# Kernel tuning notes

Hardware: AMD Instinct MI355X
Metric: run time of the kernel (lower is better)

Reference implementation:

```python
import jax, jax.numpy as jnp
import numpy as np

B, S, D = 256, 512, 256
ATT = 128

def setup_inputs() -> dict:
    key = jax.random.key(0)
    k1, k2, k3, k4 = jax.random.split(key, 4)
    x = jax.random.normal(k1, (B, S, D), dtype=jnp.float32)
    W = jax.random.normal(k2, (D, ATT), dtype=jnp.float32)
    b = jax.random.normal(k3, (ATT,), dtype=jnp.float32)
    u = jax.random.normal(k4, (ATT, 1), dtype=jnp.float32)
    return {"x": x, "W": W, "b": b, "u": u}

def reference(x, W, b, u):
    # uit: [B, S, ATT]
    uit = jnp.tanh(jnp.einsum('bsd,da->bsa', x, W) + b)
    # scores: [B, S]  (faithful: exp without max-subtraction, as in original)
    ait = jnp.exp(jnp.einsum('bsa,a->bs', uit, u[:, 0]))
    ait = ait / (jnp.sum(ait, axis=1, keepdims=True) + 1e-08)
    # weighted sum over seq -> [B, D]
    return jnp.einsum('bsd,bs->bd', x, ait)
```

## Files before the change

kernel.cpp:

```cpp
#include <hip/hip_runtime.h>
#include <math.h>

typedef _Float16 f16x8 __attribute__((ext_vector_type(8)));
typedef float    f32x4 __attribute__((ext_vector_type(4)));

constexpr int B_ = 256, S_ = 512, D_ = 256, A_ = 128;
constexpr int BS = B_ * S_;

constexpr size_t WH_OFF = (size_t)BS * sizeof(float);
constexpr size_t WL_OFF = WH_OFF + (size_t)D_ * A_ * 2;

__global__ __launch_bounds__(256) void k_packW(const float* __restrict__ W,
                                               _Float16* __restrict__ Wh,
                                               _Float16* __restrict__ Wl)
{
    int tid = blockIdx.x * 256 + threadIdx.x;
    int l  = tid & 63;
    int nf = (tid >> 6) & 7;
    int ks = tid >> 9;
    int n  = nf * 16 + (l & 15);
    int k0 = ks * 32 + ((l >> 4) & 3) * 8;
    f16x8 hi, lo;
#pragma unroll
    for (int i = 0; i < 8; ++i) {
        float v = W[(k0 + i) * A_ + n];
        _Float16 h = (_Float16)v;
        hi[i] = h;
        lo[i] = (_Float16)(v - (float)h);
    }
    *(f16x8*)(Wh + (size_t)tid * 8) = hi;
    *(f16x8*)(Wl + (size_t)tid * 8) = lo;
}

__global__ __launch_bounds__(256, 2) void k_scores(
    const float* __restrict__ x, const _Float16* __restrict__ Wh,
    const _Float16* __restrict__ Wl, const float* __restrict__ bvec,
    const float* __restrict__ u, float* __restrict__ scores)
{
    const int lane = threadIdx.x & 63;
    const int wv   = threadIdx.x >> 6;
    const int row_base = blockIdx.x * 256 + wv * 64;
    const int lr = lane & 15;
    const int lg = lane >> 4;

    const f32x4 vzero = {0.f, 0.f, 0.f, 0.f};
    f32x4 acc[4][8];
#pragma unroll
    for (int mf = 0; mf < 4; ++mf)
#pragma unroll
        for (int nf = 0; nf < 8; ++nf) acc[mf][nf] = vzero;

    for (int ks = 0; ks < 8; ++ks) {
        f16x8 ah[4], al[4];
#pragma unroll
        for (int mf = 0; mf < 4; ++mf) {
            const float* xp = x + (size_t)(row_base + mf * 16 + lr) * D_ + ks * 32 + lg * 8;
            float4 v0 = *(const float4*)xp;
            float4 v1 = *(const float4*)(xp + 4);
            f16x8 h, lo;
            h[0] = (_Float16)v0.x; h[1] = (_Float16)v0.y;
            h[2] = (_Float16)v0.z; h[3] = (_Float16)v0.w;
            h[4] = (_Float16)v1.x; h[5] = (_Float16)v1.y;
            h[6] = (_Float16)v1.z; h[7] = (_Float16)v1.w;
            lo[0] = (_Float16)(v0.x - (float)h[0]); lo[1] = (_Float16)(v0.y - (float)h[1]);
            lo[2] = (_Float16)(v0.z - (float)h[2]); lo[3] = (_Float16)(v0.w - (float)h[3]);
            lo[4] = (_Float16)(v1.x - (float)h[4]); lo[5] = (_Float16)(v1.y - (float)h[5]);
            lo[6] = (_Float16)(v1.z - (float)h[6]); lo[7] = (_Float16)(v1.w - (float)h[7]);
            ah[mf] = h; al[mf] = lo;
        }
        const f16x8* WhB = (const f16x8*)Wh + (size_t)ks * 8 * 64 + lane;
        const f16x8* WlB = (const f16x8*)Wl + (size_t)ks * 8 * 64 + lane;
#pragma unroll
        for (int nf = 0; nf < 8; ++nf) {
            f16x8 bh = WhB[nf * 64];
            f16x8 bl = WlB[nf * 64];
#pragma unroll
            for (int mf = 0; mf < 4; ++mf) {
                acc[mf][nf] = __builtin_amdgcn_mfma_f32_16x16x32_f16(ah[mf], bh, acc[mf][nf], 0, 0, 0);
                acc[mf][nf] = __builtin_amdgcn_mfma_f32_16x16x32_f16(ah[mf], bl, acc[mf][nf], 0, 0, 0);
                acc[mf][nf] = __builtin_amdgcn_mfma_f32_16x16x32_f16(al[mf], bh, acc[mf][nf], 0, 0, 0);
            }
        }
    }

    float bb[8], uu[8];
#pragma unroll
    for (int nf = 0; nf < 8; ++nf) {
        bb[nf] = bvec[nf * 16 + lr];
        uu[nf] = u[nf * 16 + lr];
    }
#pragma unroll
    for (int mf = 0; mf < 4; ++mf) {
#pragma unroll
        for (int r = 0; r < 4; ++r) {
            float s = 0.f;
#pragma unroll
            for (int nf = 0; nf < 8; ++nf)
                s += tanhf(acc[mf][nf][r] + bb[nf]) * uu[nf];
#pragma unroll
            for (int m = 8; m >= 1; m >>= 1)
                s += __shfl_xor(s, m, 64);
            if (lr == 0)
                scores[row_base + mf * 16 + lg * 4 + r] = expf(s);
        }
    }
}

__global__ __launch_bounds__(512) void k_out(
    const float* __restrict__ x, const float* __restrict__ scores,
    float* __restrict__ out)
{
    __shared__ float sc[S_];
    __shared__ float red[8];
    __shared__ float pbuf[8][D_];

    const int t = threadIdx.x, b = blockIdx.x;
    const int lane = t & 63, w = t >> 6;

    float v = scores[(size_t)b * S_ + t];
    sc[t] = v;
    float rv = v;
#pragma unroll
    for (int m = 32; m >= 1; m >>= 1) rv += __shfl_xor(rv, m, 64);
    if (lane == 0) red[w] = rv;
    __syncthreads();

    const float* xp = x + ((size_t)b * S_ + (size_t)w * 64) * D_ + lane * 4;
    float4 a0 = {0.f, 0.f, 0.f, 0.f}, a1 = {0.f, 0.f, 0.f, 0.f};
#pragma unroll 8
    for (int j = 0; j < 64; j += 2) {
        float4 xa = *(const float4*)(xp + (size_t)j * D_);
        float4 xb = *(const float4*)(xp + (size_t)(j + 1) * D_);
        float s0 = sc[w * 64 + j], s1 = sc[w * 64 + j + 1];
        a0.x = fmaf(xa.x, s0, a0.x); a0.y = fmaf(xa.y, s0, a0.y);
        a0.z = fmaf(xa.z, s0, a0.z); a0.w = fmaf(xa.w, s0, a0.w);
        a1.x = fmaf(xb.x, s1, a1.x); a1.y = fmaf(xb.y, s1, a1.y);
        a1.z = fmaf(xb.z, s1, a1.z); a1.w = fmaf(xb.w, s1, a1.w);
    }
    float4 asum = {a0.x + a1.x, a0.y + a1.y, a0.z + a1.z, a0.w + a1.w};
    *(float4*)(&pbuf[w][lane * 4]) = asum;
    __syncthreads();

    if (t < D_) {
        float denom = 0.f;
#pragma unroll
        for (int i = 0; i < 8; ++i) denom += red[i];
        const float inv = 1.0f / (denom + 1e-8f);
        float r = 0.f;
#pragma unroll
        for (int w2 = 0; w2 < 8; ++w2) r += pbuf[w2][t];
        out[b * D_ + t] = r * inv;
    }
}

extern "C" void kernel_launch(void* const* d_in, const int* in_sizes, int n_in,
                              void* d_out, int out_size, void* d_ws, size_t ws_size,
                              hipStream_t stream)
{
    const float* x    = (const float*)d_in[0];
    const float* W    = (const float*)d_in[1];
    const float* bvec = (const float*)d_in[2];
    const float* u    = (const float*)d_in[3];
    float* out = (float*)d_out;

    float*    scores = (float*)d_ws;
    _Float16* Wh     = (_Float16*)((char*)d_ws + WH_OFF);
    _Float16* Wl     = (_Float16*)((char*)d_ws + WL_OFF);

    k_packW <<<16, 256, 0, stream>>>(W, Wh, Wl);
    k_scores<<<BS / 256, 256, 0, stream>>>(x, Wh, Wl, bvec, u, scores);
    k_out   <<<B_, 512, 0, stream>>>(x, scores, out);
}
```

Measured before the change: 253.0 us.

## Keep W fragments in registers, stage x tiles through LDS with prefetch

The scores kernel now keeps each wave's W hi/lo fragments resident in registers. Each wave owns two column fragments and loops over 32-row tiles of x, which are split into fp16 hi/lo and staged through double-synchronised LDS. Global loads for the next tile are issued before the MFMA work on the current one, and per-wave partial dot products are combined through shared memory. tanhf is replaced with an exp-based fast tanh, and k_out is widened to 1024 threads with half the rows per wave, which adds register pressure and more barriers in exchange.

```diff
diff --git a/kernel.cpp b/kernel.cpp
--- a/kernel.cpp
+++ b/kernel.cpp
@@ -9,6 +9,10 @@
 
 constexpr size_t WH_OFF = (size_t)BS * sizeof(float);
 constexpr size_t WL_OFF = WH_OFF + (size_t)D_ * A_ * 2;
+
+__device__ __forceinline__ float tanh_fast(float v) {
+    return 1.0f - 2.0f / (1.0f + __expf(2.0f * v));
+}
 
 __global__ __launch_bounds__(256) void k_packW(const float* __restrict__ W,
                                                _Float16* __restrict__ Wh,
@@ -37,108 +41,159 @@
     const _Float16* __restrict__ Wl, const float* __restrict__ bvec,
     const float* __restrict__ u, float* __restrict__ scores)
 {
-    const int lane = threadIdx.x & 63;
-    const int wv   = threadIdx.x >> 6;
-    const int row_base = blockIdx.x * 256 + wv * 64;
-    const int lr = lane & 15;
-    const int lg = lane >> 4;
-
-    const f32x4 vzero = {0.f, 0.f, 0.f, 0.f};
-    f32x4 acc[4][8];
-#pragma unroll
-    for (int mf = 0; mf < 4; ++mf)
-#pragma unroll
-        for (int nf = 0; nf < 8; ++nf) acc[mf][nf] = vzero;
-
-    for (int ks = 0; ks < 8; ++ks) {
-        f16x8 ah[4], al[4];
-#pragma unroll
-        for (int mf = 0; mf < 4; ++mf) {
-            const float* xp = x + (size_t)(row_base + mf * 16 + lr) * D_ + ks * 32 + lg * 8;
-            float4 v0 = *(const float4*)xp;
-            float4 v1 = *(const float4*)(xp + 4);
-            f16x8 h, lo;
-            h[0] = (_Float16)v0.x; h[1] = (_Float16)v0.y;
-            h[2] = (_Float16)v0.z; h[3] = (_Float16)v0.w;
-            h[4] = (_Float16)v1.x; h[5] = (_Float16)v1.y;
-            h[6] = (_Float16)v1.z; h[7] = (_Float16)v1.w;
-            lo[0] = (_Float16)(v0.x - (float)h[0]); lo[1] = (_Float16)(v0.y - (float)h[1]);
-            lo[2] = (_Float16)(v0.z - (float)h[2]); lo[3] = (_Float16)(v0.w - (float)h[3]);
-            lo[4] = (_Float16)(v1.x - (float)h[4]); lo[5] = (_Float16)(v1.y - (float)h[5]);
-            lo[6] = (_Float16)(v1.z - (float)h[6]); lo[7] = (_Float16)(v1.w - (float)h[7]);
-            ah[mf] = h; al[mf] = lo;
-        }
-        const f16x8* WhB = (const f16x8*)Wh + (size_t)ks * 8 * 64 + lane;
-        const f16x8* WlB = (const f16x8*)Wl + (size_t)ks * 8 * 64 + lane;
-#pragma unroll
-        for (int nf = 0; nf < 8; ++nf) {
-            f16x8 bh = WhB[nf * 64];
-            f16x8 bl = WlB[nf * 64];
-#pragma unroll
-            for (int mf = 0; mf < 4; ++mf) {
-                acc[mf][nf] = __builtin_amdgcn_mfma_f32_16x16x32_f16(ah[mf], bh, acc[mf][nf], 0, 0, 0);
-                acc[mf][nf] = __builtin_amdgcn_mfma_f32_16x16x32_f16(ah[mf], bl, acc[mf][nf], 0, 0, 0);
-                acc[mf][nf] = __builtin_amdgcn_mfma_f32_16x16x32_f16(al[mf], bh, acc[mf][nf], 0, 0, 0);
-            }
-        }
-    }
-
-    float bb[8], uu[8];
-#pragma unroll
-    for (int nf = 0; nf < 8; ++nf) {
-        bb[nf] = bvec[nf * 16 + lr];
-        uu[nf] = u[nf * 16 + lr];
-    }
-#pragma unroll
-    for (int mf = 0; mf < 4; ++mf) {
-#pragma unroll
-        for (int r = 0; r < 4; ++r) {
-            float s = 0.f;
-#pragma unroll
-            for (int nf = 0; nf < 8; ++nf)
-                s += tanhf(acc[mf][nf][r] + bb[nf]) * uu[nf];
-#pragma unroll
-            for (int m = 8; m >= 1; m >>= 1)
-                s += __shfl_xor(s, m, 64);
-            if (lr == 0)
-                scores[row_base + mf * 16 + lg * 4 + r] = expf(s);
-        }
-    }
-}
-
-__global__ __launch_bounds__(512) void k_out(
+    __shared__ _Float16 xh[16 * 64 * 8];
+    __shared__ _Float16 xl[16 * 64 * 8];
+    __shared__ float    part[2][4][32];
+
+    const int t    = threadIdx.x;
+    const int lane = t & 63, wv = t >> 6;
+    const int lr   = lane & 15, lg = lane >> 4;
+    const int brow0 = blockIdx.x * 256;
+
+    f16x8 Bh[8][2], Bl[8][2];
+#pragma unroll
+    for (int ks = 0; ks < 8; ++ks)
+#pragma unroll
+        for (int j = 0; j < 2; ++j) {
+            int nf = wv * 2 + j;
+            Bh[ks][j] = *(const f16x8*)(Wh + ((size_t)(ks * 8 + nf) * 64 + lane) * 8);
+            Bl[ks][j] = *(const f16x8*)(Wl + ((size_t)(ks * 8 + nf) * 64 + lane) * 8);
+        }
+
+    const float bb0 = bvec[(wv * 2 + 0) * 16 + lr], uu0 = u[(wv * 2 + 0) * 16 + lr];
+    const float bb1 = bvec[(wv * 2 + 1) * 16 + lr], uu1 = u[(wv * 2 + 1) * 16 + lr];
+
+    float4 ld[4][2];
+
+#pragma unroll
+    for (int it = 0; it < 4; ++it) {
+        int f = wv * 4 + it;
+        const float* p = x + (size_t)(brow0 + ((f >> 3) << 4) + lr) * D_
+                           + ((f & 7) << 5) + (lg << 3);
+        ld[it][0] = *(const float4*)p;
+        ld[it][1] = *(const float4*)(p + 4);
+    }
+#pragma unroll
+    for (int it = 0; it < 4; ++it) {
+        int f = wv * 4 + it;
+        float v[8] = {ld[it][0].x, ld[it][0].y, ld[it][0].z, ld[it][0].w,
+                      ld[it][1].x, ld[it][1].y, ld[it][1].z, ld[it][1].w};
+        f16x8 hi, lo;
+#pragma unroll
+        for (int i = 0; i < 8; ++i) {
+            _Float16 h = (_Float16)v[i];
+            hi[i] = h; lo[i] = (_Float16)(v[i] - (float)h);
+        }
+        *(f16x8*)&xh[((size_t)f * 64 + lane) * 8] = hi;
+        *(f16x8*)&xl[((size_t)f * 64 + lane) * 8] = lo;
+    }
+
+    for (int tt = 0; tt < 8; ++tt) {
+        __syncthreads();
+        if (tt > 0 && t < 32) {
+            int pp = (tt - 1) & 1;
+            float ss = part[pp][0][t] + part[pp][1][t] + part[pp][2][t] + part[pp][3][t];
+            scores[brow0 + (tt - 1) * 32 + t] = __expf(ss);
+        }
+        if (tt < 7) {
+#pragma unroll
+            for (int it = 0; it < 4; ++it) {
+                int f = wv * 4 + it;
+                const float* p = x + (size_t)(brow0 + (tt + 1) * 32 + ((f >> 3) << 4) + lr) * D_
+                                   + ((f & 7) << 5) + (lg << 3);
+                ld[it][0] = *(const float4*)p;
+                ld[it][1] = *(const float4*)(p + 4);
+            }
+        }
+        f32x4 acc[2][2];
+#pragma unroll
+        for (int mt = 0; mt < 2; ++mt)
+#pragma unroll
+            for (int j = 0; j < 2; ++j) acc[mt][j] = (f32x4){0.f, 0.f, 0.f, 0.f};
+#pragma unroll
+        for (int mt = 0; mt < 2; ++mt)
+#pragma unroll
+            for (int ks = 0; ks < 8; ++ks) {
+                int fi = mt * 8 + ks;
+                f16x8 ah = *(const f16x8*)&xh[((size_t)fi * 64 + lane) * 8];
+                f16x8 al = *(const f16x8*)&xl[((size_t)fi * 64 + lane) * 8];
+                acc[mt][0] = __builtin_amdgcn_mfma_f32_16x16x32_f16(ah, Bh[ks][0], acc[mt][0], 0, 0, 0);
+                acc[mt][0] = __builtin_amdgcn_mfma_f32_16x16x32_f16(ah, Bl[ks][0], acc[mt][0], 0, 0, 0);
+                acc[mt][0] = __builtin_amdgcn_mfma_f32_16x16x32_f16(al, Bh[ks][0], acc[mt][0], 0, 0, 0);
+                acc[mt][1] = __builtin_amdgcn_mfma_f32_16x16x32_f16(ah, Bh[ks][1], acc[mt][1], 0, 0, 0);
+                acc[mt][1] = __builtin_amdgcn_mfma_f32_16x16x32_f16(ah, Bl[ks][1], acc[mt][1], 0, 0, 0);
+                acc[mt][1] = __builtin_amdgcn_mfma_f32_16x16x32_f16(al, Bh[ks][1], acc[mt][1], 0, 0, 0);
+            }
+        const int par = tt & 1;
+#pragma unroll
+        for (int mt = 0; mt < 2; ++mt)
+#pragma unroll
+            for (int r = 0; r < 4; ++r) {
+                float s = tanh_fast(acc[mt][0][r] + bb0) * uu0
+                        + tanh_fast(acc[mt][1][r] + bb1) * uu1;
+                s += __shfl_xor(s, 8, 64);
+                s += __shfl_xor(s, 4, 64);
+                s += __shfl_xor(s, 2, 64);
+                s += __shfl_xor(s, 1, 64);
+                if (lr == 0) part[par][wv][mt * 16 + lg * 4 + r] = s;
+            }
+        __syncthreads();
+        if (tt < 7) {
+#pragma unroll
+            for (int it = 0; it < 4; ++it) {
+                int f = wv * 4 + it;
+                float v[8] = {ld[it][0].x, ld[it][0].y, ld[it][0].z, ld[it][0].w,
+                              ld[it][1].x, ld[it][1].y, ld[it][1].z, ld[it][1].w};
+                f16x8 hi, lo;
+#pragma unroll
+                for (int i = 0; i < 8; ++i) {
+                    _Float16 h = (_Float16)v[i];
+                    hi[i] = h; lo[i] = (_Float16)(v[i] - (float)h);
+                }
+                *(f16x8*)&xh[((size_t)f * 64 + lane) * 8] = hi;
+                *(f16x8*)&xl[((size_t)f * 64 + lane) * 8] = lo;
+            }
+        }
+    }
+    __syncthreads();
+    if (t < 32) {
+        float ss = part[1][0][t] + part[1][1][t] + part[1][2][t] + part[1][3][t];
+        scores[brow0 + 7 * 32 + t] = __expf(ss);
+    }
+}
+
+__global__ __launch_bounds__(1024) void k_out(
     const float* __restrict__ x, const float* __restrict__ scores,
     float* __restrict__ out)
 {
     __shared__ float sc[S_];
     __shared__ float red[8];
-    __shared__ float pbuf[8][D_];
+    __shared__ float pbuf[16][D_];
 
     const int t = threadIdx.x, b = blockIdx.x;
     const int lane = t & 63, w = t >> 6;
 
-    float v = scores[(size_t)b * S_ + t];
-    sc[t] = v;
-    float rv = v;
-#pragma unroll
-    for (int m = 32; m >= 1; m >>= 1) rv += __shfl_xor(rv, m, 64);
-    if (lane == 0) red[w] = rv;
+    if (t < S_) {
+        float v = scores[(size_t)b * S_ + t];
+        sc[t] = v;
+#pragma unroll
+        for (int m = 32; m >= 1; m >>= 1) v += __shfl_xor(v, m, 64);
+        if (lane == 0) red[w] = v;
+    }
     __syncthreads();
 
-    const float* xp = x + ((size_t)b * S_ + (size_t)w * 64) * D_ + lane * 4;
-    float4 a0 = {0.f, 0.f, 0.f, 0.f}, a1 = {0.f, 0.f, 0.f, 0.f};
+    const float* xp = x + ((size_t)b * S_ + (size_t)w * 32) * D_ + lane * 4;
+    f32x4 a = {0.f, 0.f, 0.f, 0.f};
 #pragma unroll 8
-    for (int j = 0; j < 64; j += 2) {
-        float4 xa = *(const float4*)(xp + (size_t)j * D_);
-        float4 xb = *(const float4*)(xp + (size_t)(j + 1) * D_);
-        float s0 = sc[w * 64 + j], s1 = sc[w * 64 + j + 1];
-        a0.x = fmaf(xa.x, s0, a0.x); a0.y = fmaf(xa.y, s0, a0.y);
-        a0.z = fmaf(xa.z, s0, a0.z); a0.w = fmaf(xa.w, s0, a0.w);
-        a1.x = fmaf(xb.x, s1, a1.x); a1.y = fmaf(xb.y, s1, a1.y);
-        a1.z = fmaf(xb.z, s1, a1.z); a1.w = fmaf(xb.w, s1, a1.w);
-    }
-    float4 asum = {a0.x + a1.x, a0.y + a1.y, a0.z + a1.z, a0.w + a1.w};
-    *(float4*)(&pbuf[w][lane * 4]) = asum;
+    for (int j = 0; j < 32; ++j) {
+        float4 xv = *(const float4*)(xp + (size_t)j * D_);
+        float s = sc[w * 32 + j];
+        a[0] = fmaf(xv.x, s, a[0]);
+        a[1] = fmaf(xv.y, s, a[1]);
+        a[2] = fmaf(xv.z, s, a[2]);
+        a[3] = fmaf(xv.w, s, a[3]);
+    }
+    *(f32x4*)&pbuf[w][lane * 4] = a;
     __syncthreads();
 
     if (t < D_) {
@@ -148,7 +203,7 @@
         const float inv = 1.0f / (denom + 1e-8f);
         float r = 0.f;
 #pragma unroll
-        for (int w2 = 0; w2 < 8; ++w2) r += pbuf[w2][t];
+        for (int i = 0; i < 16; ++i) r += pbuf[i][t];
         out[b * D_ + t] = r * inv;
     }
 }
@@ -168,6 +223,6 @@
     _Float16* Wl     = (_Float16*)((char*)d_ws + WL_OFF);
 
     k_packW <<<16, 256, 0, stream>>>(W, Wh, Wl);
-    k_scores<<<BS / 256, 256, 0, stream>>>(x, Wh, Wl, bvec, u, scores);
-    k_out   <<<B_, 512, 0, stream>>>(x, scores, out);
-}
+    k_scores<<<512, 256, 0, stream>>>(x, Wh, Wl, bvec, u, scores);
+    k_out   <<<B_, 1024, 0, stream>>>(x, scores, out);
+}
```

Result: faster. 226.1 us (-10.6%).

## Keep W fragments in registers, stage x via LDS with pipelined prefetch

Applied to the files above, without the earlier changes.

Drops the separate W packing kernel. Each wave of k_scores now splits W into fp16 hi/lo fragments in registers for its own 16 attention columns. Blocks of 512 threads loop over 8 tiles of 32 rows: each tile of x is converted once to hi/lo fp16 and staged in shared memory so all 8 waves reuse it, and the next tile's global loads are issued while the MFMAs run. Per-wave partial scores are reduced across waves through double-buffered shared memory, and tanhf is replaced with an exp-based approximation. This trades extra block syncs and some tanh accuracy for much less per-wave x reloading and conversion, and fewer accumulator registers.

```diff
diff --git a/kernel.cpp b/kernel.cpp
--- a/kernel.cpp
+++ b/kernel.cpp
@@ -7,103 +7,121 @@
 constexpr int B_ = 256, S_ = 512, D_ = 256, A_ = 128;
 constexpr int BS = B_ * S_;
 
-constexpr size_t WH_OFF = (size_t)BS * sizeof(float);
-constexpr size_t WL_OFF = WH_OFF + (size_t)D_ * A_ * 2;
-
-__global__ __launch_bounds__(256) void k_packW(const float* __restrict__ W,
-                                               _Float16* __restrict__ Wh,
-                                               _Float16* __restrict__ Wl)
-{
-    int tid = blockIdx.x * 256 + threadIdx.x;
-    int l  = tid & 63;
-    int nf = (tid >> 6) & 7;
-    int ks = tid >> 9;
-    int n  = nf * 16 + (l & 15);
-    int k0 = ks * 32 + ((l >> 4) & 3) * 8;
-    f16x8 hi, lo;
-#pragma unroll
-    for (int i = 0; i < 8; ++i) {
-        float v = W[(k0 + i) * A_ + n];
-        _Float16 h = (_Float16)v;
-        hi[i] = h;
-        lo[i] = (_Float16)(v - (float)h);
-    }
-    *(f16x8*)(Wh + (size_t)tid * 8) = hi;
-    *(f16x8*)(Wl + (size_t)tid * 8) = lo;
+__device__ __forceinline__ float tanh_fast(float v) {
+    return 1.0f - 2.0f / (1.0f + __expf(2.0f * v));
 }
 
-__global__ __launch_bounds__(256, 2) void k_scores(
-    const float* __restrict__ x, const _Float16* __restrict__ Wh,
-    const _Float16* __restrict__ Wl, const float* __restrict__ bvec,
-    const float* __restrict__ u, float* __restrict__ scores)
+__global__ __launch_bounds__(512, 4) void k_scores(
+    const float* __restrict__ x, const float* __restrict__ W,
+    const float* __restrict__ bvec, const float* __restrict__ u,
+    float* __restrict__ scores)
 {
-    const int lane = threadIdx.x & 63;
-    const int wv   = threadIdx.x >> 6;
-    const int row_base = blockIdx.x * 256 + wv * 64;
-    const int lr = lane & 15;
-    const int lg = lane >> 4;
+    __shared__ _Float16 xh[16 * 64 * 8];
+    __shared__ _Float16 xl[16 * 64 * 8];
+    __shared__ float    part[2][8][32];
 
-    const f32x4 vzero = {0.f, 0.f, 0.f, 0.f};
-    f32x4 acc[4][8];
+    const int t    = threadIdx.x;
+    const int lane = t & 63, wv = t >> 6;
+    const int lr   = lane & 15, lg = lane >> 4;
+    const int brow0 = blockIdx.x * 256;
+
+    f16x8 Bh[8], Bl[8];
 #pragma unroll
-    for (int mf = 0; mf < 4; ++mf)
+    for (int ks = 0; ks < 8; ++ks) {
+        const float* wp = W + (size_t)(ks * 32 + lg * 8) * A_ + wv * 16 + lr;
 #pragma unroll
-        for (int nf = 0; nf < 8; ++nf) acc[mf][nf] = vzero;
+        for (int i = 0; i < 8; ++i) {
+            float v = wp[(size_t)i * A_];
+            _Float16 h = (_Float16)v;
+            Bh[ks][i] = h;
+            Bl[ks][i] = (_Float16)(v - (float)h);
+        }
+    }
+    const float bb = bvec[wv * 16 + lr];
+    const float uu = u[wv * 16 + lr];
 
-    for (int ks = 0; ks < 8; ++ks) {
-        f16x8 ah[4], al[4];
+    float4 ld[2][2];
+
+#define K1_ISSUE(TT)                                                              \
+    {                                                                             \
+        _Pragma("unroll")                                                         \
+        for (int ff = 0; ff < 2; ++ff) {                                          \
+            int f = wv * 2 + ff;                                                  \
+            const float* p = x + (size_t)(brow0 + (TT) * 32 + ((f >> 3) << 4) + lr) * D_ \
+                               + ((f & 7) << 5) + (lg << 3);                      \
+            ld[ff][0] = *(const float4*)p;                                        \
+            ld[ff][1] = *(const float4*)(p + 4);                                  \
+        }                                                                         \
+    }
+
+#define K1_STAGE()                                                                \
+    {                                                                             \
+        _Pragma("unroll")                                                         \
+        for (int ff = 0; ff < 2; ++ff) {                                          \
+            int f = wv * 2 + ff;                                                  \
+            float v[8] = {ld[ff][0].x, ld[ff][0].y, ld[ff][0].z, ld[ff][0].w,     \
+                          ld[ff][1].x, ld[ff][1].y, ld[ff][1].z, ld[ff][1].w};    \
+            f16x8 hi, lo;                                                         \
+            _Pragma("unroll")                                                     \
+            for (int i = 0; i < 8; ++i) {                                         \
+                _Float16 h = (_Float16)v[i];                                      \
+                hi[i] = h; lo[i] = (_Float16)(v[i] - (float)h);                   \
+            }                                                                     \
+            *(f16x8*)&xh[((size_t)f * 64 + lane) * 8] = hi;                       \
+            *(f16x8*)&xl[((size_t)f * 64 + lane) * 8] = lo;                       \
+        }                                                                         \
+    }
+
+    K1_ISSUE(0)
+    K1_STAGE()
+
+    for (int tt = 0; tt < 8; ++tt) {
+        __syncthreads();
+        if (tt > 0 && t < 32) {
+            const float* pp = &part[(tt - 1) & 1][0][t];
+            float ss = pp[0] + pp[32] + pp[64] + pp[96] + pp[128] + pp[160] + pp[192] + pp[224];
+            scores[brow0 + (tt - 1) * 32 + t] = __expf(ss);
+        }
+        if (tt < 7) K1_ISSUE(tt + 1)
+
+        f32x4 acc0 = {0.f, 0.f, 0.f, 0.f}, acc1 = {0.f, 0.f, 0.f, 0.f};
 #pragma unroll
-        for (int mf = 0; mf < 4; ++mf) {
-            const float* xp = x + (size_t)(row_base + mf * 16 + lr) * D_ + ks * 32 + lg * 8;
-            float4 v0 = *(const float4*)xp;
-            float4 v1 = *(const float4*)(xp + 4);
-            f16x8 h, lo;
-            h[0] = (_Float16)v0.x; h[1] = (_Float16)v0.y;
-            h[2] = (_Float16)v0.z; h[3] = (_Float16)v0.w;
-            h[4] = (_Float16)v1.x; h[5] = (_Float16)v1.y;
-            h[6] = (_Float16)v1.z; h[7] = (_Float16)v1.w;
-            lo[0] = (_Float16)(v0.x - (float)h[0]); lo[1] = (_Float16)(v0.y - (float)h[1]);
-            lo[2] = (_Float16)(v0.z - (float)h[2]); lo[3] = (_Float16)(v0.w - (float)h[3]);
-            lo[4] = (_Float16)(v1.x - (float)h[4]); lo[5] = (_Float16)(v1.y - (float)h[5]);
-            lo[6] = (_Float16)(v1.z - (float)h[6]); lo[7] = (_Float16)(v1.w - (float)h[7]);
-            ah[mf] = h; al[mf] = lo;
+        for (int ks = 0; ks < 8; ++ks) {
+            f16x8 ah0 = *(const f16x8*)&xh[((size_t)(ks) * 64 + lane) * 8];
+            f16x8 al0 = *(const f16x8*)&xl[((size_t)(ks) * 64 + lane) * 8];
+            f16x8 ah1 = *(const f16x8*)&xh[((size_t)(8 + ks) * 64 + lane) * 8];
+            f16x8 al1 = *(const f16x8*)&xl[((size_t)(8 + ks) * 64 + lane) * 8];
+            acc0 = __builtin_amdgcn_mfma_f32_16x16x32_f16(ah0, Bh[ks], acc0, 0, 0, 0);
+            acc0 = __builtin_amdgcn_mfma_f32_16x16x32_f16(ah0, Bl[ks], acc0, 0, 0, 0);
+            acc0 = __builtin_amdgcn_mfma_f32_16x16x32_f16(al0, Bh[ks], acc0, 0, 0, 0);
+            acc1 = __builtin_amdgcn_mfma_f32_16x16x32_f16(ah1, Bh[ks], acc1, 0, 0, 0);
+            acc1 = __builtin_amdgcn_mfma_f32_16x16x32_f16(ah1, Bl[ks], acc1, 0, 0, 0);
+            acc1 = __builtin_amdgcn_mfma_f32_16x16x32_f16(al1, Bh[ks], acc1, 0, 0, 0);
         }
-        const f16x8* WhB = (const f16x8*)Wh + (size_t)ks * 8 * 64 + lane;
-        const f16x8* WlB = (const f16x8*)Wl + (size_t)ks * 8 * 64 + lane;
 #pragma unroll
-        for (int nf = 0; nf < 8; ++nf) {
-            f16x8 bh = WhB[nf * 64];
-            f16x8 bl = WlB[nf * 64];
+        for (int mt = 0; mt < 2; ++mt) {
+            f32x4 a = mt ? acc1 : acc0;
 #pragma unroll
-            for (int mf = 0; mf < 4; ++mf) {
-                acc[mf][nf] = __builtin_amdgcn_mfma_f32_16x16x32_f16(ah[mf], bh, acc[mf][nf], 0, 0, 0);
-                acc[mf][nf] = __builtin_amdgcn_mfma_f32_16x16x32_f16(ah[mf], bl, acc[mf][nf], 0, 0, 0);
-                acc[mf][nf] = __builtin_amdgcn_mfma_f32_16x16x32_f16(al[mf], bh, acc[mf][nf], 0, 0, 0);
+            for (int r = 0; r < 4; ++r) {
+                float s = tanh_fast(a[r] + bb) * uu;
+                s += __shfl_xor(s, 8, 64);
+                s += __shfl_xor(s, 4, 64);
+                s += __shfl_xor(s, 2, 64);
+                s += __shfl_xor(s, 1, 64);
+                if (lr == 0) part[tt & 1][wv][mt * 16 + lg * 4 + r] = s;
             }
         }
+        __syncthreads();
+        if (tt < 7) K1_STAGE()
     }
-
-    float bb[8], uu[8];
-#pragma unroll
-    for (int nf = 0; nf < 8; ++nf) {
-        bb[nf] = bvec[nf * 16 + lr];
-        uu[nf] = u[nf * 16 + lr];
+    __syncthreads();
+    if (t < 32) {
+        const float* pp = &part[1][0][t];
+        float ss = pp[0] + pp[32] + pp[64] + pp[96] + pp[128] + pp[160] + pp[192] + pp[224];
+        scores[brow0 + 7 * 32 + t] = __expf(ss);
     }
-#pragma unroll
-    for (int mf = 0; mf < 4; ++mf) {
-#pragma unroll
-        for (int r = 0; r < 4; ++r) {
-            float s = 0.f;
-#pragma unroll
-            for (int nf = 0; nf < 8; ++nf)
-                s += tanhf(acc[mf][nf][r] + bb[nf]) * uu[nf];
-#pragma unroll
-            for (int m = 8; m >= 1; m >>= 1)
-                s += __shfl_xor(s, m, 64);
-            if (lr == 0)
-                scores[row_base + mf * 16 + lg * 4 + r] = expf(s);
-        }
-    }
+#undef K1_ISSUE
+#undef K1_STAGE
 }
 
 __global__ __launch_bounds__(512) void k_out(
@@ -126,19 +144,19 @@
     __syncthreads();
 
     const float* xp = x + ((size_t)b * S_ + (size_t)w * 64) * D_ + lane * 4;
-    float4 a0 = {0.f, 0.f, 0.f, 0.f}, a1 = {0.f, 0.f, 0.f, 0.f};
+    f32x4 a0 = {0.f, 0.f, 0.f, 0.f}, a1 = {0.f, 0.f, 0.f, 0.f};
 #pragma unroll 8
     for (int j = 0; j < 64; j += 2) {
         float4 xa = *(const float4*)(xp + (size_t)j * D_);
         float4 xb = *(const float4*)(xp + (size_t)(j + 1) * D_);
         float s0 = sc[w * 64 + j], s1 = sc[w * 64 + j + 1];
-        a0.x = fmaf(xa.x, s0, a0.x); a0.y = fmaf(xa.y, s0, a0.y);
-        a0.z = fmaf(xa.z, s0, a0.z); a0.w = fmaf(xa.w, s0, a0.w);
-        a1.x = fmaf(xb.x, s1, a1.x); a1.y = fmaf(xb.y, s1, a1.y);
-        a1.z = fmaf(xb.z, s1, a1.z); a1.w = fmaf(xb.w, s1, a1.w);
+        a0[0] = fmaf(xa.x, s0, a0[0]); a0[1] = fmaf(xa.y, s0, a0[1]);
+        a0[2] = fmaf(xa.z, s0, a0[2]); a0[3] = fmaf(xa.w, s0, a0[3]);
+        a1[0] = fmaf(xb.x, s1, a1[0]); a1[1] = fmaf(xb.y, s1, a1[1]);
+        a1[2] = fmaf(xb.z, s1, a1[2]); a1[3] = fmaf(xb.w, s1, a1[3]);
     }
-    float4 asum = {a0.x + a1.x, a0.y + a1.y, a0.z + a1.z, a0.w + a1.w};
-    *(float4*)(&pbuf[w][lane * 4]) = asum;
+    a0[0] += a1[0]; a0[1] += a1[1]; a0[2] += a1[2]; a0[3] += a1[3];
+    *(f32x4*)&pbuf[w][lane * 4] = a0;
     __syncthreads();
 
     if (t < D_) {
@@ -148,7 +166,7 @@
         const float inv = 1.0f / (denom + 1e-8f);
         float r = 0.f;
 #pragma unroll
-        for (int w2 = 0; w2 < 8; ++w2) r += pbuf[w2][t];
+        for (int i = 0; i < 8; ++i) r += pbuf[i][t];
         out[b * D_ + t] = r * inv;
     }
 }
@@ -162,12 +180,8 @@
     const float* bvec = (const float*)d_in[2];
     const float* u    = (const float*)d_in[3];
     float* out = (float*)d_out;
+    float* scores = (float*)d_ws;
 
-    float*    scores = (float*)d_ws;
-    _Float16* Wh     = (_Float16*)((char*)d_ws + WH_OFF);
-    _Float16* Wl     = (_Float16*)((char*)d_ws + WL_OFF);
-
-    k_packW <<<16, 256, 0, stream>>>(W, Wh, Wl);
-    k_scores<<<BS / 256, 256, 0, stream>>>(x, Wh, Wl, bvec, u, scores);
+    k_scores<<<512, 512, 0, stream>>>(x, W, bvec, u, scores);
     k_out   <<<B_, 512, 0, stream>>>(x, scores, out);
 }
```

Result: faster. 224.5 us (-11.3%).
